# Kernel optimization log

Hardware: AMD Instinct MI355X
Metric: run time of the kernel (lower is better)

## Reference

```python
import jax, jax.numpy as jnp
import numpy as np

N = 262144   # query points
M = 4096     # boundary points
D = 128      # d_model (m)
H = 4        # num_heads
HD = D // H  # head_dim = 32
L = 3        # num_layers
PI = float(np.pi)


def multi_feature_encoding(x):
    # x: [T, 2] -> [T, 30]; 15 fixed feature maps, hstacked
    feats = [
        x,
        x ** 2,
        (x - 1.5) ** 2,
        (x - 4.5) ** 2,
        jax.nn.sigmoid(x),
        jax.nn.sigmoid(x - 1.5),
        jax.nn.sigmoid(x - 4.5),
        x - 1.5,
        x - 4.5,
        jnp.sin(PI * x),
        jnp.cos(PI * x),
        jnp.sin(PI * x * 0.25),
        jnp.cos(PI * x * 0.25),
        jnp.sin(PI * x * 0.5),
        jnp.cos(PI * x * 0.5),
    ]
    return jnp.concatenate(feats, axis=-1)


def pos_encode(x, w, b):
    # w: [30, D], b: [D]
    return jnp.sin(multi_feature_encoding(x) @ w + b)


def setup_inputs() -> dict:
    key = jax.random.key(0)
    ks = jax.random.split(key, 24)
    s = 0.05

    def p(k, shape):
        return jax.random.normal(k, shape, dtype=jnp.float32) * s

    return {
        "query_pts": jax.random.normal(ks[0], (N, 2), dtype=jnp.float32),
        "boundary_pts": jax.random.normal(ks[1], (M, 2), dtype=jnp.float32),
        # positional encoders (query / boundary)
        "pe_w": p(ks[2], (30, D)), "pe_b": p(ks[3], (D,)),
        "bpe_w": p(ks[4], (30, D)), "bpe_b": p(ks[5], (D,)),
        # per-layer per-head q/k/v projections, stacked: [L, H, D, HD]
        "Wq": p(ks[6], (L, H, D, HD)), "bq": p(ks[7], (L, H, HD)),
        "Wk": p(ks[8], (L, H, D, HD)), "bk": p(ks[9], (L, H, HD)),
        "Wv": p(ks[10], (L, H, D, HD)), "bv": p(ks[11], (L, H, HD)),
        # attention out proj and FFN (two D->D linears) per layer
        "Wo": p(ks[12], (L, D, D)), "bo": p(ks[13], (L, D)),
        "W1": p(ks[14], (L, D, D)), "b1": p(ks[15], (L, D)),
        "W2": p(ks[16], (L, D, D)), "b2": p(ks[17], (L, D)),
        # final projector: D -> D//2 -> 3
        "pw1": p(ks[18], (D, D // 2)), "pb1": p(ks[19], (D // 2,)),
        "pw2": p(ks[20], (D // 2, 3)), "pb2": p(ks[21], (3,)),
    }


def reference(query_pts, boundary_pts, pe_w, pe_b, bpe_w, bpe_b,
              Wq, bq, Wk, bk, Wv, bv, Wo, bo, W1, b1, W2, b2,
              pw1, pb1, pw2, pb2):
    h = pos_encode(query_pts, pe_w, pe_b)[None]        # [1, N, D]
    b_enc = pos_encode(boundary_pts, bpe_w, bpe_b)[None]  # [1, M, D]

    for l in range(L):
        # batched per-head projections (equivalent to the per-head Linear loop)
        qh = jnp.einsum('btd,hde->bhte', h, Wq[l]) + bq[l][None, :, None, :]
        kh = jnp.einsum('btd,hde->bhte', b_enc, Wk[l]) + bk[l][None, :, None, :]
        vh = jnp.einsum('btd,hde->bhte', b_enc, Wv[l]) + bv[l][None, :, None, :]
        qh = qh ** 2  # squared feature map
        kh = kh ** 2
        kv_sum = jnp.einsum('bhnd,bhne->bhde', kh, vh)          # [1,H,HD,HD]
        z = 1.0 / (jnp.einsum('bhnd,bhd->bhn', qh, kh.sum(axis=2)) + 1e-6)
        attn = jnp.einsum('bhnd,bhde,bhn->bhne', qh, kv_sum, z)  # [1,H,N,HD]
        attn = attn.transpose(0, 2, 1, 3).reshape(1, -1, D)      # [1,N,D]
        attn = attn @ Wo[l] + bo[l]
        x = h + attn
        ff = jax.nn.gelu(x @ W1[l] + b1[l], approximate=False) @ W2[l] + b2[l]
        h = x + ff

    out = jax.nn.gelu(h @ pw1 + pb1, approximate=False) @ pw2 + pb2  # [1,N,3]
    return out[0]  # squeeze(0) -> [N, 3]
```

## Files before the change

### kernel.cpp

```cpp
#include <hip/hip_runtime.h>
#include <hip/hip_bf16.h>

__device__ __forceinline__ float b2f(unsigned short u) {
    return __uint_as_float(((unsigned)u) << 16);
}
__device__ __forceinline__ unsigned short f2b(float f) {
    __hip_bfloat16 h = __float2bfloat16(f);
    return *reinterpret_cast<unsigned short*>(&h);
}
__device__ __forceinline__ unsigned short f2b_rne(float f) {
    unsigned u = __float_as_uint(f);
    return (unsigned short)((u + 0x7fffu + ((u >> 16) & 1u)) >> 16);
}
__device__ __forceinline__ unsigned pk_bf16(float lo, float hi) {
    unsigned r;
    asm("v_cvt_pk_bf16_f32 %0, %1, %2" : "=v"(r) : "v"(lo), "v"(hi));
    return r;
}
__device__ __forceinline__ float sigm(float v) {
    return 1.f / (1.f + __expf(-v));
}
__device__ __forceinline__ float gelu_t(float x) {
    float y = 0.7978845608f * (x + 0.044715f * x * x * x);
    float e = __expf(2.f * y);
    float th = 1.f - 2.f / (e + 1.f);
    return 0.5f * x * (1.f + th);
}

typedef __attribute__((ext_vector_type(8))) short s8v;
typedef __attribute__((ext_vector_type(4))) float f4v;

#define MFMA_BF16 __builtin_amdgcn_mfma_f32_16x16x32_bf16

__device__ __forceinline__ void make_feats(const unsigned short* __restrict__ qpts,
                                           int r, float* __restrict__ f) {
    unsigned pq = *(const unsigned*)(qpts + (size_t)r * 2);
    float x0 = b2f((unsigned short)(pq & 0xffff));
    float x1 = b2f((unsigned short)(pq >> 16));
    const float PI = 3.14159265358979323846f;
    float a0 = x0 - 1.5f, a1 = x1 - 1.5f, c0 = x0 - 4.5f, c1 = x1 - 4.5f;
    f[0] = x0;        f[1] = x1;
    f[2] = x0 * x0;   f[3] = x1 * x1;
    f[4] = a0 * a0;   f[5] = a1 * a1;
    f[6] = c0 * c0;   f[7] = c1 * c1;
    f[8] = sigm(x0);  f[9] = sigm(x1);
    f[10] = sigm(a0); f[11] = sigm(a1);
    f[12] = sigm(c0); f[13] = sigm(c1);
    f[14] = a0;       f[15] = a1;
    f[16] = c0;       f[17] = c1;
    f[18] = __sinf(PI * x0);          f[19] = __sinf(PI * x1);
    f[20] = __cosf(PI * x0);          f[21] = __cosf(PI * x1);
    f[22] = __sinf(PI * 0.25f * x0);  f[23] = __sinf(PI * 0.25f * x1);
    f[24] = __cosf(PI * 0.25f * x0);  f[25] = __cosf(PI * 0.25f * x1);
    f[26] = __sinf(PI * 0.5f * x0);   f[27] = __sinf(PI * 0.5f * x1);
    f[28] = __cosf(PI * 0.5f * x0);   f[29] = __cosf(PI * 0.5f * x1);
}

__device__ __forceinline__ void feats8(unsigned pq, int qd, float* __restrict__ f8) {
    float x0 = b2f((unsigned short)(pq & 0xffff));
    float x1 = b2f((unsigned short)(pq >> 16));
    const float PI = 3.14159265358979323846f;
    float a0 = x0 - 1.5f, a1 = x1 - 1.5f, c0 = x0 - 4.5f, c1 = x1 - 4.5f;
    if (qd == 0) {
        f8[0] = x0;      f8[1] = x1;
        f8[2] = x0 * x0; f8[3] = x1 * x1;
        f8[4] = a0 * a0; f8[5] = a1 * a1;
        f8[6] = c0 * c0; f8[7] = c1 * c1;
    } else if (qd == 1) {
        f8[0] = sigm(x0); f8[1] = sigm(x1);
        f8[2] = sigm(a0); f8[3] = sigm(a1);
        f8[4] = sigm(c0); f8[5] = sigm(c1);
        f8[6] = a0;       f8[7] = a1;
    } else if (qd == 2) {
        f8[0] = c0; f8[1] = c1;
        f8[2] = __sinf(PI * x0);          f8[3] = __sinf(PI * x1);
        f8[4] = __cosf(PI * x0);          f8[5] = __cosf(PI * x1);
        f8[6] = __sinf(PI * 0.25f * x0);  f8[7] = __sinf(PI * 0.25f * x1);
    } else {
        f8[0] = __cosf(PI * 0.25f * x0);  f8[1] = __cosf(PI * 0.25f * x1);
        f8[2] = __sinf(PI * 0.5f * x0);   f8[3] = __sinf(PI * 0.5f * x1);
        f8[4] = __cosf(PI * 0.5f * x0);   f8[5] = __cosf(PI * 0.5f * x1);
        f8[6] = 0.f;                      f8[7] = 0.f;
    }
}

struct ConvArgs {
    const void* p[22];
    int off[23];
};

__global__ __launch_bounds__(256) void convert_kernel(
    ConvArgs a, const unsigned short* __restrict__ pe_w_raw,
    int* __restrict__ flag, unsigned short* __restrict__ canon, int total)
{
    __shared__ int cnt;
    if (threadIdx.x == 0) cnt = 0;
    __syncthreads();
    float v = b2f(pe_w_raw[threadIdx.x * 2]);
    if (!(fabsf(v) < 1.0f)) atomicAdd(&cnt, 1);
    __syncthreads();
    int isf32 = (cnt >= 16) ? 1 : 0;
    if (blockIdx.x == 0 && threadIdx.x == 0) *flag = isf32;

    int g = blockIdx.x * 256 + threadIdx.x;
    if (g >= total) return;
    int s = 0;
    #pragma unroll
    for (int i = 1; i < 23; i++) s += (g >= a.off[i]) ? 1 : 0;
    int local = g - a.off[s];
    unsigned short r;
    if (isf32) r = f2b(((const float*)a.p[s])[local]);
    else       r = ((const unsigned short*)a.p[s])[local];
    canon[g] = r;
}

__global__ __launch_bounds__(256) void encode_kernel(
    const unsigned short* __restrict__ pts,
    const unsigned short* __restrict__ w,
    const unsigned short* __restrict__ b,
    float* __restrict__ out)
{
    __shared__ __align__(16) float wsm[30 * 128];
    __shared__ float bs[128];
    int t = threadIdx.x;
    for (int i = t; i < 30 * 128; i += 256) wsm[i] = b2f(w[i]);
    if (t < 128) bs[t] = b2f(b[t]);
    __syncthreads();

    int r = blockIdx.x * 8 + (t >> 5);
    int j = t & 31;
    float f[30];
    make_feats(pts, r, f);
    float s0 = bs[j * 4 + 0], s1 = bs[j * 4 + 1], s2 = bs[j * 4 + 2], s3 = bs[j * 4 + 3];
    #pragma unroll
    for (int ff = 0; ff < 30; ff++) {
        float4 wv = *(const float4*)&wsm[ff * 128 + j * 4];
        float fv = f[ff];
        s0 += fv * wv.x; s1 += fv * wv.y; s2 += fv * wv.z; s3 += fv * wv.w;
    }
    *(float4*)&out[(size_t)r * 128 + j * 4] =
        make_float4(__sinf(s0), __sinf(s1), __sinf(s2), __sinf(s3));
}

__global__ __launch_bounds__(256) void khvh_kernel(
    const float* __restrict__ benc,
    const unsigned short* __restrict__ Wk, const unsigned short* __restrict__ bk,
    const unsigned short* __restrict__ Wv, const unsigned short* __restrict__ bv,
    float* __restrict__ kh, float* __restrict__ vh, float* __restrict__ kvz)
{
    int g = blockIdx.x * 256 + threadIdx.x;
    if (g < 12672) kvz[g] = 0.f;
    int lh = g >> 17;
    int rem = g & 131071;
    int m = rem >> 5;
    int dd = rem & 31;
    const unsigned short* wk = Wk + lh * 4096 + dd;
    const unsigned short* wv = Wv + lh * 4096 + dd;
    const float* br = benc + (size_t)m * 128;
    float ka = 0.f, va = 0.f;
    #pragma unroll 8
    for (int c = 0; c < 128; c++) {
        float bb = br[c];
        ka += bb * b2f(wk[c * 32]);
        va += bb * b2f(wv[c * 32]);
    }
    ka += b2f(bk[lh * 32 + dd]); ka = ka * ka;
    va += b2f(bv[lh * 32 + dd]);
    kh[g] = ka; vh[g] = va;
}

__global__ __launch_bounds__(1024) void kvred_kernel(
    const float* __restrict__ kh, const float* __restrict__ vh,
    float* __restrict__ kvsum, float* __restrict__ ksum)
{
    __shared__ float khs[1024];
    __shared__ float vhs[1024];
    int t = threadIdx.x;
    int lh = blockIdx.x >> 3;
    int part = blockIdx.x & 7;
    int dd = t >> 5, ee = t & 31;
    float kva = 0.f, ksa = 0.f;
    for (int ch = 0; ch < 16; ch++) {
        int base = lh * 131072 + (part * 16 + ch) * 1024;
        khs[t] = kh[base + t];
        vhs[t] = vh[base + t];
        __syncthreads();
        #pragma unroll
        for (int i = 0; i < 32; i++) {
            float kk = khs[i * 32 + dd];
            kva += kk * vhs[i * 32 + ee];
            ksa += kk;
        }
        __syncthreads();
    }
    atomicAdd(&kvsum[lh * 1024 + dd * 32 + ee], kva);
    if (ee == 0) atomicAdd(&ksum[lh * 32 + dd], ksa);
}

__global__ __launch_bounds__(256) void prep_kernel(
    const unsigned short* __restrict__ Wq, const unsigned short* __restrict__ W1,
    const unsigned short* __restrict__ W2, const unsigned short* __restrict__ pw1,
    const float* __restrict__ kvs, const float* __restrict__ kss,
    const unsigned short* __restrict__ Wo, const unsigned short* __restrict__ pe_w,
    unsigned short* __restrict__ wqT, unsigned short* __restrict__ w1T,
    unsigned short* __restrict__ w2T, unsigned short* __restrict__ pw1T,
    unsigned short* __restrict__ waT, unsigned short* __restrict__ ksT,
    unsigned short* __restrict__ pweT)
{
    int g = blockIdx.x * 256 + threadIdx.x;
    if (g < 49152) {
        int l = g >> 14, r = g & 16383, n = r >> 7, k = r & 127;
        wqT[g] = Wq[((l * 4 + (n >> 5)) * 128 + k) * 32 + (n & 31)];
    } else if (g < 98304) {
        int q = g - 49152; int l = q >> 14, r = q & 16383, n = r >> 7, k = r & 127;
        w1T[q] = W1[(l * 128 + k) * 128 + n];
    } else if (g < 147456) {
        int q = g - 98304; int l = q >> 14, r = q & 16383, n = r >> 7, k = r & 127;
        w2T[q] = W2[(l * 128 + k) * 128 + n];
    } else if (g < 155648) {
        int q = g - 147456; int n = q >> 7, k = q & 127;
        pw1T[q] = pw1[k * 64 + n];
    } else if (g < 204800) {
        int q = g - 155648; int l = q >> 14, r = q & 16383, n = r >> 7, k = r & 127;
        int hk = k >> 5, dk = k & 31;
        const float* kvp = kvs + (l * 4 + hk) * 1024 + dk * 32;
        const unsigned short* wop = Wo + (size_t)(l * 128 + hk * 32) * 128 + n;
        float s = 0.f;
        #pragma unroll 8
        for (int j = 0; j < 32; j++) s += kvp[j] * b2f(wop[j * 128]);
        waT[q] = f2b(s);
    } else if (g < 210944) {
        int q = g - 204800; int l = q >> 11, r = q & 2047, n = r >> 7, k = r & 127;
        unsigned short v = 0;
        if (n < 4 && (k >> 5) == n) v = f2b(kss[(l * 4 + n) * 32 + (k & 31)]);
        ksT[q] = v;
    } else if (g < 215040) {
        int q = g - 210944; int n = q >> 5, k = q & 31;
        pweT[q] = (k < 30) ? pe_w[k * 128 + n] : (unsigned short)0;
    }
}


template<int ITERS>
__device__ __forceinline__ void stage_w(const unsigned short* __restrict__ g,
                                        unsigned short* __restrict__ wbuf, int t) {
    #pragma unroll
    for (int i = 0; i < ITERS; i++) {
        int lin = (i * 256 + t) * 16;
        s8v v = *(const s8v*)((const char*)g + lin);
        int sw = lin ^ ((((lin >> 8)) & 7) << 4);
        *(s8v*)((char*)wbuf + sw) = v;
    }
}

__device__ __forceinline__ s8v wfrag(const unsigned short* __restrict__ wbuf,
                                     int nt, int k, int l16, int qd) {
    int lin = (nt << 12) + (l16 << 8) + (k << 6) + (qd << 4);
    return *(const s8v*)((const char*)wbuf + (lin ^ ((l16 & 7) << 4)));
}

#define RUN_MM_L(AF, ...) do {                                                \
    _Pragma("unroll")                                                         \
    for (int _p = 0; _p < 4; _p++) {                                          \
        f4v _x0 = {0.f,0.f,0.f,0.f}, _x1 = {0.f,0.f,0.f,0.f};                 \
        f4v _y0 = {0.f,0.f,0.f,0.f}, _y1 = {0.f,0.f,0.f,0.f};                 \
        _Pragma("unroll")                                                     \
        for (int _k = 0; _k < 4; _k++) {                                      \
            s8v _wa = wfrag(wbuf, _p * 2,     _k, l16, qd);                   \
            s8v _wb = wfrag(wbuf, _p * 2 + 1, _k, l16, qd);                   \
            _x0 = MFMA_BF16(_wa, AF[0][_k], _x0, 0, 0, 0);                    \
            _x1 = MFMA_BF16(_wa, AF[1][_k], _x1, 0, 0, 0);                    \
            _y0 = MFMA_BF16(_wb, AF[0][_k], _y0, 0, 0, 0);                    \
            _y1 = MFMA_BF16(_wb, AF[1][_k], _y1, 0, 0, 0);                    \
        }                                                                     \
        { const int nt = _p * 2;     const int tile = 0; const f4v x = _x0; __VA_ARGS__ } \
        { const int nt = _p * 2;     const int tile = 1; const f4v x = _x1; __VA_ARGS__ } \
        { const int nt = _p * 2 + 1; const int tile = 0; const f4v x = _y0; __VA_ARGS__ } \
        { const int nt = _p * 2 + 1; const int tile = 1; const f4v x = _y1; __VA_ARGS__ } \
    }                                                                         \
} while (0)

#define LOAD_AF(AF) do {                                                      \
    _Pragma("unroll")                                                         \
    for (int _t2 = 0; _t2 < 2; _t2++)                                         \
        _Pragma("unroll")                                                     \
        for (int _k = 0; _k < 4; _k++)                                        \
            AF[_t2][_k] = *(const s8v*)(sAB + (rA0 + _t2 * 16) * 256 +        \
                                        (((_k * 64) + (qd * 16)) ^ swzA));    \
} while (0)

__global__ __launch_bounds__(256) void mega_kernel(
    const unsigned short* __restrict__ qpts,
    const unsigned short* __restrict__ pweT,
    const unsigned short* __restrict__ pe_b,
    const unsigned short* __restrict__ wqT,
    const unsigned short* __restrict__ waT,
    const unsigned short* __restrict__ ksT,
    const unsigned short* __restrict__ w1T,
    const unsigned short* __restrict__ w2T,
    const unsigned short* __restrict__ bq,
    const unsigned short* __restrict__ bo,
    const unsigned short* __restrict__ b1,
    const unsigned short* __restrict__ b2,
    const unsigned short* __restrict__ pw1T,
    const unsigned short* __restrict__ pb1,
    const unsigned short* __restrict__ pw2,
    const unsigned short* __restrict__ pb2,
    void* __restrict__ outv, const int* __restrict__ flag)
{
    __shared__ __align__(16) unsigned short sA[128 * 128];
    __shared__ __align__(16) unsigned short wbuf[16384];
    __shared__ __align__(16) float biasAll[12 * 128];
    __shared__ __align__(16) float pebs[128];
    __shared__ __align__(16) float pb1s[64];
    __shared__ float w2s[192];
    __shared__ float pb2s[3];

    int t = threadIdx.x;
    int wvi = t >> 6, ln = t & 63, qd = ln >> 4, l16 = ln & 15;
    int qd4 = qd * 4;
    int row0 = blockIdx.x * 128;
    int rA0 = wvi * 32 + l16;
    const int swzA = (l16 & 7) << 4;
    char* sAB = (char*)sA;

    for (int i = t; i < 1536; i += 256) {
        int l = i >> 9, rem = i & 511, which = rem >> 7, c = rem & 127;
        const unsigned short* bsrc = (which == 0) ? bq : (which == 1) ? bo
                                   : (which == 2) ? b1 : b2;
        biasAll[i] = b2f(bsrc[l * 128 + c]);
    }
    if (t < 128) pebs[t] = b2f(pe_b[t]);
    if (t < 64)  pb1s[t] = b2f(pb1[t]);
    if (t < 192) w2s[t] = b2f(pw2[t]);
    if (t < 3)   pb2s[t] = b2f(pb2[t]);
    __syncthreads();

    stage_w<8>(wqT, wbuf, t);

    float hres[2][8][4];

    {
        unsigned pq0 = *(const unsigned*)(qpts + (size_t)(row0 + rA0) * 2);
        unsigned pq1 = *(const unsigned*)(qpts + (size_t)(row0 + rA0 + 16) * 2);
        s8v ae0, ae1;
        {
            float f8[8]; feats8(pq0, qd, f8);
            unsigned* au = (unsigned*)&ae0;
            #pragma unroll
            for (int jj = 0; jj < 4; jj++) au[jj] = pk_bf16(f8[2 * jj], f8[2 * jj + 1]);
        }
        {
            float f8[8]; feats8(pq1, qd, f8);
            unsigned* au = (unsigned*)&ae1;
            #pragma unroll
            for (int jj = 0; jj < 4; jj++) au[jj] = pk_bf16(f8[2 * jj], f8[2 * jj + 1]);
        }
        const unsigned short* pb = pweT + l16 * 32 + qd * 8;
        #pragma unroll
        for (int nt = 0; nt < 8; nt++) {
            s8v aw = *(const s8v*)(pb + nt * 512);
            f4v x0 = {0.f, 0.f, 0.f, 0.f}, x1 = {0.f, 0.f, 0.f, 0.f};
            x0 = MFMA_BF16(aw, ae0, x0, 0, 0, 0);
            x1 = MFMA_BF16(aw, ae1, x1, 0, 0, 0);
            float4 bb = *(const float4*)&pebs[nt * 16 + qd4];
            float h0 = __sinf(x0[0] + bb.x), h1 = __sinf(x0[1] + bb.y);
            float h2 = __sinf(x0[2] + bb.z), h3 = __sinf(x0[3] + bb.w);
            hres[0][nt][0] = h0; hres[0][nt][1] = h1;
            hres[0][nt][2] = h2; hres[0][nt][3] = h3;
            uint2 pk0; pk0.x = pk_bf16(h0, h1); pk0.y = pk_bf16(h2, h3);
            *(uint2*)(sAB + rA0 * 256 + ((nt * 32 + qd * 8) ^ swzA)) = pk0;
            float g0 = __sinf(x1[0] + bb.x), g1 = __sinf(x1[1] + bb.y);
            float g2 = __sinf(x1[2] + bb.z), g3 = __sinf(x1[3] + bb.w);
            hres[1][nt][0] = g0; hres[1][nt][1] = g1;
            hres[1][nt][2] = g2; hres[1][nt][3] = g3;
            uint2 pk1; pk1.x = pk_bf16(g0, g1); pk1.y = pk_bf16(g2, g3);
            *(uint2*)(sAB + (rA0 + 16) * 256 + ((nt * 32 + qd * 8) ^ swzA)) = pk1;
        }
    }

    s8v af[2][4];

    for (int l = 0; l < 3; l++) {
        const float* bql = &biasAll[(l * 4 + 0) * 128];
        const float* bol = &biasAll[(l * 4 + 1) * 128];
        const float* b1l = &biasAll[(l * 4 + 2) * 128];
        const float* b2l = &biasAll[(l * 4 + 3) * 128];

        LOAD_AF(af);
        __syncthreads();
        if (l > 0) {  }
        RUN_MM_L(af, {
            float4 bb = *(const float4*)&bql[nt * 16 + qd4];
            float v0 = x[0] + bb.x, v1 = x[1] + bb.y;
            float v2 = x[2] + bb.z, v3 = x[3] + bb.w;
            uint2 pk; pk.x = pk_bf16(v0 * v0, v1 * v1); pk.y = pk_bf16(v2 * v2, v3 * v3);
            *(uint2*)(sAB + (rA0 + tile * 16) * 256 + ((nt * 32 + qd * 8) ^ swzA)) = pk;
        });

        LOAD_AF(af);
        s8v kf[4];
        {
            const unsigned short* kb = ksT + l * 2048 + l16 * 128 + qd * 8;
            #pragma unroll
            for (int ks = 0; ks < 4; ks++) kf[ks] = *(const s8v*)(kb + ks * 32);
        }
        __syncthreads();
        stage_w<8>(waT + l * 16384, wbuf, t);
        #pragma unroll
        for (int tile = 0; tile < 2; tile++) {
            f4v d = {0.f, 0.f, 0.f, 0.f};
            #pragma unroll
            for (int ks = 0; ks < 4; ks++) d = MFMA_BF16(kf[ks], af[tile][ks], d, 0, 0, 0);
            #pragma unroll
            for (int ks = 0; ks < 4; ks++) {
                float z = 1.f / (__shfl(d[ks], l16) + 1e-6f);
                unsigned* u = (unsigned*)&af[tile][ks];
                #pragma unroll
                for (int jj = 0; jj < 4; jj++) {
                    unsigned w = u[jj];
                    float lo = __uint_as_float(w << 16) * z;
                    float hi = __uint_as_float(w & 0xffff0000u) * z;
                    u[jj] = pk_bf16(lo, hi);
                }
            }
        }
        __syncthreads();

        RUN_MM_L(af, {
            float4 bb = *(const float4*)&bol[nt * 16 + qd4];
            float v0 = hres[tile][nt][0] + x[0] + bb.x;
            float v1 = hres[tile][nt][1] + x[1] + bb.y;
            float v2 = hres[tile][nt][2] + x[2] + bb.z;
            float v3 = hres[tile][nt][3] + x[3] + bb.w;
            hres[tile][nt][0] = v0; hres[tile][nt][1] = v1;
            hres[tile][nt][2] = v2; hres[tile][nt][3] = v3;
            uint2 pk; pk.x = pk_bf16(v0, v1); pk.y = pk_bf16(v2, v3);
            *(uint2*)(sAB + (rA0 + tile * 16) * 256 + ((nt * 32 + qd * 8) ^ swzA)) = pk;
        });

        LOAD_AF(af);
        __syncthreads();
        stage_w<8>(w1T + l * 16384, wbuf, t);
        __syncthreads();
        RUN_MM_L(af, {
            float4 bb = *(const float4*)&b1l[nt * 16 + qd4];
            uint2 pk;
            pk.x = pk_bf16(gelu_t(x[0] + bb.x), gelu_t(x[1] + bb.y));
            pk.y = pk_bf16(gelu_t(x[2] + bb.z), gelu_t(x[3] + bb.w));
            *(uint2*)(sAB + (rA0 + tile * 16) * 256 + ((nt * 32 + qd * 8) ^ swzA)) = pk;
        });

        LOAD_AF(af);
        __syncthreads();
        stage_w<8>(w2T + l * 16384, wbuf, t);
        __syncthreads();
        RUN_MM_L(af, {
            float4 bb = *(const float4*)&b2l[nt * 16 + qd4];
            float v0 = hres[tile][nt][0] + x[0] + bb.x;
            float v1 = hres[tile][nt][1] + x[1] + bb.y;
            float v2 = hres[tile][nt][2] + x[2] + bb.z;
            float v3 = hres[tile][nt][3] + x[3] + bb.w;
            hres[tile][nt][0] = v0; hres[tile][nt][1] = v1;
            hres[tile][nt][2] = v2; hres[tile][nt][3] = v3;
            uint2 pk; pk.x = pk_bf16(v0, v1); pk.y = pk_bf16(v2, v3);
            *(uint2*)(sAB + (rA0 + tile * 16) * 256 + ((nt * 32 + qd * 8) ^ swzA)) = pk;
        });

        LOAD_AF(af);
        __syncthreads();
        if (l < 2) stage_w<8>(wqT + (l + 1) * 16384, wbuf, t);
        else       stage_w<4>(pw1T, wbuf, t);
    }

    __syncthreads();
    {
        float* sAf = (float*)sA;
        const int fsw = (l16 & 7) << 1;
        #pragma unroll
        for (int p = 0; p < 2; p++) {
            f4v y0 = {0.f,0.f,0.f,0.f}, y1 = {0.f,0.f,0.f,0.f};
            f4v y2 = {0.f,0.f,0.f,0.f}, y3 = {0.f,0.f,0.f,0.f};
            #pragma unroll
            for (int ks = 0; ks < 4; ks++) {
                s8v wA = wfrag(wbuf, p * 2,     ks, l16, qd);
                s8v wB = wfrag(wbuf, p * 2 + 1, ks, l16, qd);
                y0 = MFMA_BF16(wA, af[0][ks], y0, 0, 0, 0);
                y1 = MFMA_BF16(wA, af[1][ks], y1, 0, 0, 0);
                y2 = MFMA_BF16(wB, af[0][ks], y2, 0, 0, 0);
                y3 = MFMA_BF16(wB, af[1][ks], y3, 0, 0, 0);
            }
            int n0 = (p * 2) * 16 + qd4, n1 = (p * 2 + 1) * 16 + qd4;
            float4 bA = *(const float4*)&pb1s[n0];
            float4 bB = *(const float4*)&pb1s[n1];
            int f0 = ((p * 2) * 4 + qd) ^ fsw, f1 = ((p * 2 + 1) * 4 + qd) ^ fsw;
            *(float4*)&sAf[rA0 * 64 + f0 * 4] = make_float4(
                gelu_t(y0[0] + bA.x), gelu_t(y0[1] + bA.y),
                gelu_t(y0[2] + bA.z), gelu_t(y0[3] + bA.w));
            *(float4*)&sAf[(rA0 + 16) * 64 + f0 * 4] = make_float4(
                gelu_t(y1[0] + bA.x), gelu_t(y1[1] + bA.y),
                gelu_t(y1[2] + bA.z), gelu_t(y1[3] + bA.w));
            *(float4*)&sAf[rA0 * 64 + f1 * 4] = make_float4(
                gelu_t(y2[0] + bB.x), gelu_t(y2[1] + bB.y),
                gelu_t(y2[2] + bB.z), gelu_t(y2[3] + bB.w));
            *(float4*)&sAf[(rA0 + 16) * 64 + f1 * 4] = make_float4(
                gelu_t(y3[0] + bB.x), gelu_t(y3[1] + bB.y),
                gelu_t(y3[2] + bB.z), gelu_t(y3[3] + bB.w));
        }
    }
    __syncthreads();

    {
        const float* sAf = (const float*)sA;
        for (int idx = t; idx < 384; idx += 256) {
            int r = idx / 3, c = idx - r * 3;
            int rsw = (r & 7) << 1;
            float s = pb2s[c];
            #pragma unroll
            for (int jj = 0; jj < 16; jj++) {
                float4 v = *(const float4*)&sAf[r * 64 + (jj ^ rsw) * 4];
                s += v.x * w2s[(jj * 4 + 0) * 3 + c] + v.y * w2s[(jj * 4 + 1) * 3 + c]
                   + v.z * w2s[(jj * 4 + 2) * 3 + c] + v.w * w2s[(jj * 4 + 3) * 3 + c];
            }
            size_t o = (size_t)(row0 + r) * 3 + c;
            if (*flag) ((float*)outv)[o] = s;
            else       ((unsigned short*)outv)[o] = f2b(s);
        }
    }
}

extern "C" void kernel_launch(void* const* d_in, const int* in_sizes, int n_in,
                              void* d_out, int out_size, void* d_ws, size_t ws_size,
                              hipStream_t stream) {
    const int N = in_sizes[0] / 2;
    const int M = in_sizes[1] / 2;

    ConvArgs ca;
    int total = 0;
    for (int i = 0; i < 22; i++) { ca.p[i] = d_in[i]; ca.off[i] = total; total += in_sizes[i]; }
    ca.off[22] = total;

    float* ws = (float*)d_ws;
    int* flag = (int*)ws;
    unsigned short* canon = (unsigned short*)(ws + 16);
    size_t canonF = ((size_t)(total + 1) / 2 + 15) & ~(size_t)15;
    float* b_enc = ws + 16 + canonF;
    float* khb   = b_enc + (size_t)M * 128;
    float* vhb   = khb + (size_t)12 * M * 32;
    float* kvs   = vhb + (size_t)12 * M * 32;
    float* kss   = kvs + 12288;
    unsigned short* wqT  = (unsigned short*)(kss + 384);
    unsigned short* waT  = wqT + 49152;
    unsigned short* w1T  = waT + 49152;
    unsigned short* w2T  = w1T + 49152;
    unsigned short* ksT  = w2T + 49152;
    unsigned short* pw1T = ksT + 6144;
    unsigned short* pweT = pw1T + 8192;

    const unsigned short* c_qpts = canon + ca.off[0];
    const unsigned short* c_bpts = canon + ca.off[1];
    const unsigned short* c_pew  = canon + ca.off[2];
    const unsigned short* c_peb  = canon + ca.off[3];
    const unsigned short* c_bpew = canon + ca.off[4];
    const unsigned short* c_bpeb = canon + ca.off[5];
    const unsigned short* c_Wq   = canon + ca.off[6];
    const unsigned short* c_bq   = canon + ca.off[7];
    const unsigned short* c_Wk   = canon + ca.off[8];
    const unsigned short* c_bk   = canon + ca.off[9];
    const unsigned short* c_Wv   = canon + ca.off[10];
    const unsigned short* c_bv   = canon + ca.off[11];
    const unsigned short* c_Wo   = canon + ca.off[12];
    const unsigned short* c_bo   = canon + ca.off[13];
    const unsigned short* c_W1   = canon + ca.off[14];
    const unsigned short* c_b1   = canon + ca.off[15];
    const unsigned short* c_W2   = canon + ca.off[16];
    const unsigned short* c_b2   = canon + ca.off[17];
    const unsigned short* c_pw1  = canon + ca.off[18];
    const unsigned short* c_pb1  = canon + ca.off[19];
    const unsigned short* c_pw2  = canon + ca.off[20];
    const unsigned short* c_pb2  = canon + ca.off[21];

    convert_kernel<<<(total + 255) / 256, 256, 0, stream>>>(
        ca, (const unsigned short*)d_in[2], flag, canon, total);

    encode_kernel<<<M / 8, 256, 0, stream>>>(c_bpts, c_bpew, c_bpeb, b_enc);
    khvh_kernel<<<(12 * M * 32) / 256, 256, 0, stream>>>(
        b_enc, c_Wk, c_bk, c_Wv, c_bv, khb, vhb, kvs);
    kvred_kernel<<<96, 1024, 0, stream>>>(khb, vhb, kvs, kss);
    prep_kernel<<<215040 / 256, 256, 0, stream>>>(
        c_Wq, c_W1, c_W2, c_pw1, kvs, kss, c_Wo, c_pew,
        wqT, w1T, w2T, pw1T, waT, ksT, pweT);

    mega_kernel<<<N / 128, 256, 0, stream>>>(
        c_qpts, pweT, c_peb, wqT, waT, ksT, w1T, w2T,
        c_bq, c_bo, c_b1, c_b2, pw1T, c_pb1, c_pw2, c_pb2, d_out, flag);
}
```

Baseline: 421.4 us.

## Keep activations in registers by permuting weight columns to match MFMA fragments

The weight output columns are permuted in the prep kernel (fmap) so each MFMA accumulator layout lines up directly with the B-operand fragment layout of the next matmul. Activations then stay packed in registers between layers instead of going through a shared-memory tile with its extra barriers. Weight staging becomes a global-to-register prefetch that overlaps compute before the LDS write. The final projector is fused into register FMAs plus cross-lane shuffles, and GELU switches to a cheaper sigmoid-form tanh approximation. The risks are higher register pressure, which can lower occupancy, and a small numerical change from the new GELU form.

```diff
diff --git a/kernel.cpp b/kernel.cpp
--- a/kernel.cpp
+++ b/kernel.cpp
@@ -7,10 +7,6 @@
 __device__ __forceinline__ unsigned short f2b(float f) {
     __hip_bfloat16 h = __float2bfloat16(f);
     return *reinterpret_cast<unsigned short*>(&h);
-}
-__device__ __forceinline__ unsigned short f2b_rne(float f) {
-    unsigned u = __float_as_uint(f);
-    return (unsigned short)((u + 0x7fffu + ((u >> 16) & 1u)) >> 16);
 }
 __device__ __forceinline__ unsigned pk_bf16(float lo, float hi) {
     unsigned r;
@@ -20,17 +16,28 @@
 __device__ __forceinline__ float sigm(float v) {
     return 1.f / (1.f + __expf(-v));
 }
-__device__ __forceinline__ float gelu_t(float x) {
-    float y = 0.7978845608f * (x + 0.044715f * x * x * x);
-    float e = __expf(2.f * y);
-    float th = 1.f - 2.f / (e + 1.f);
-    return 0.5f * x * (1.f + th);
+__device__ __forceinline__ float gelu_l(float x) {
+    float x2 = x * x;
+    float y2 = x * __builtin_fmaf(0.0713548163f, x2, 1.5957691216f);
+    float e  = __expf(y2);
+    float r  = __builtin_amdgcn_rcpf(e + 1.f);
+    return x - x * r;
 }
 
 typedef __attribute__((ext_vector_type(8))) short s8v;
 typedef __attribute__((ext_vector_type(4))) float f4v;
 
 #define MFMA_BF16 __builtin_amdgcn_mfma_f32_16x16x32_bf16
+
+__device__ __forceinline__ s8v mkfrag(unsigned a, unsigned b, unsigned c, unsigned d) {
+    union { unsigned u[4]; s8v v; } x;
+    x.u[0] = a; x.u[1] = b; x.u[2] = c; x.u[3] = d;
+    return x.v;
+}
+
+__device__ __forceinline__ int fmap(int s) {
+    return (s & ~31) | (((s >> 2) & 3) << 3) | (((s >> 4) & 1) << 2) | (s & 3);
+}
 
 __device__ __forceinline__ void make_feats(const unsigned short* __restrict__ qpts,
                                            int r, float* __restrict__ f) {
@@ -210,21 +217,23 @@
     int g = blockIdx.x * 256 + threadIdx.x;
     if (g < 49152) {
         int l = g >> 14, r = g & 16383, n = r >> 7, k = r & 127;
-        wqT[g] = Wq[((l * 4 + (n >> 5)) * 128 + k) * 32 + (n & 31)];
+        int na = fmap(n);
+        wqT[g] = Wq[((l * 4 + (na >> 5)) * 128 + k) * 32 + (na & 31)];
     } else if (g < 98304) {
         int q = g - 49152; int l = q >> 14, r = q & 16383, n = r >> 7, k = r & 127;
-        w1T[q] = W1[(l * 128 + k) * 128 + n];
+        w1T[q] = W1[(l * 128 + k) * 128 + fmap(n)];
     } else if (g < 147456) {
         int q = g - 98304; int l = q >> 14, r = q & 16383, n = r >> 7, k = r & 127;
-        w2T[q] = W2[(l * 128 + k) * 128 + n];
+        w2T[q] = W2[(l * 128 + k) * 128 + fmap(n)];
     } else if (g < 155648) {
         int q = g - 147456; int n = q >> 7, k = q & 127;
         pw1T[q] = pw1[k * 64 + n];
     } else if (g < 204800) {
         int q = g - 155648; int l = q >> 14, r = q & 16383, n = r >> 7, k = r & 127;
+        int na = fmap(n);
         int hk = k >> 5, dk = k & 31;
         const float* kvp = kvs + (l * 4 + hk) * 1024 + dk * 32;
-        const unsigned short* wop = Wo + (size_t)(l * 128 + hk * 32) * 128 + n;
+        const unsigned short* wop = Wo + (size_t)(l * 128 + hk * 32) * 128 + na;
         float s = 0.f;
         #pragma unroll 8
         for (int j = 0; j < 32; j++) s += kvp[j] * b2f(wop[j * 128]);
@@ -236,20 +245,26 @@
         ksT[q] = v;
     } else if (g < 215040) {
         int q = g - 210944; int n = q >> 5, k = q & 31;
-        pweT[q] = (k < 30) ? pe_w[k * 128 + n] : (unsigned short)0;
+        pweT[q] = (k < 30) ? pe_w[k * 128 + fmap(n)] : (unsigned short)0;
     }
 }
 
 
 template<int ITERS>
-__device__ __forceinline__ void stage_w(const unsigned short* __restrict__ g,
-                                        unsigned short* __restrict__ wbuf, int t) {
+__device__ __forceinline__ void load_w(const unsigned short* __restrict__ g,
+                                       int t, s8v* __restrict__ r) {
+    #pragma unroll
+    for (int i = 0; i < ITERS; i++)
+        r[i] = *(const s8v*)((const char*)g + (size_t)(i * 256 + t) * 16);
+}
+template<int ITERS>
+__device__ __forceinline__ void write_w(unsigned short* __restrict__ wbuf,
+                                        int t, const s8v* __restrict__ r) {
     #pragma unroll
     for (int i = 0; i < ITERS; i++) {
         int lin = (i * 256 + t) * 16;
-        s8v v = *(const s8v*)((const char*)g + lin);
-        int sw = lin ^ ((((lin >> 8)) & 7) << 4);
-        *(s8v*)((char*)wbuf + sw) = v;
+        int sw = lin ^ (((lin >> 8) & 7) << 4);
+        *(s8v*)((char*)wbuf + sw) = r[i];
     }
 }
 
@@ -259,35 +274,35 @@
     return *(const s8v*)((const char*)wbuf + (lin ^ ((l16 & 7) << 4)));
 }
 
-#define RUN_MM_L(AF, ...) do {                                                \
+#define MM_BODY(EPI...) do {                                                  \
+    s8v bf0[4], bf1[4];                                                       \
+    _Pragma("unroll")                                                         \
+    for (int _s = 0; _s < 4; _s++) {                                          \
+        bf0[_s] = mkfrag(pkd[0][2*_s][0], pkd[0][2*_s][1],                    \
+                         pkd[0][2*_s+1][0], pkd[0][2*_s+1][1]);               \
+        bf1[_s] = mkfrag(pkd[1][2*_s][0], pkd[1][2*_s][1],                    \
+                         pkd[1][2*_s+1][0], pkd[1][2*_s+1][1]);               \
+    }                                                                         \
     _Pragma("unroll")                                                         \
     for (int _p = 0; _p < 4; _p++) {                                          \
-        f4v _x0 = {0.f,0.f,0.f,0.f}, _x1 = {0.f,0.f,0.f,0.f};                 \
-        f4v _y0 = {0.f,0.f,0.f,0.f}, _y1 = {0.f,0.f,0.f,0.f};                 \
+        f4v _x0 = {0.f,0.f,0.f,0.f}, _x1 = _x0, _y0 = _x0, _y1 = _x0;         \
         _Pragma("unroll")                                                     \
         for (int _k = 0; _k < 4; _k++) {                                      \
             s8v _wa = wfrag(wbuf, _p * 2,     _k, l16, qd);                   \
             s8v _wb = wfrag(wbuf, _p * 2 + 1, _k, l16, qd);                   \
-            _x0 = MFMA_BF16(_wa, AF[0][_k], _x0, 0, 0, 0);                    \
-            _x1 = MFMA_BF16(_wa, AF[1][_k], _x1, 0, 0, 0);                    \
-            _y0 = MFMA_BF16(_wb, AF[0][_k], _y0, 0, 0, 0);                    \
-            _y1 = MFMA_BF16(_wb, AF[1][_k], _y1, 0, 0, 0);                    \
+            _x0 = MFMA_BF16(_wa, bf0[_k], _x0, 0, 0, 0);                      \
+            _x1 = MFMA_BF16(_wa, bf1[_k], _x1, 0, 0, 0);                      \
+            _y0 = MFMA_BF16(_wb, bf0[_k], _y0, 0, 0, 0);                      \
+            _y1 = MFMA_BF16(_wb, bf1[_k], _y1, 0, 0, 0);                      \
         }                                                                     \
-        { const int nt = _p * 2;     const int tile = 0; const f4v x = _x0; __VA_ARGS__ } \
-        { const int nt = _p * 2;     const int tile = 1; const f4v x = _x1; __VA_ARGS__ } \
-        { const int nt = _p * 2 + 1; const int tile = 0; const f4v x = _y0; __VA_ARGS__ } \
-        { const int nt = _p * 2 + 1; const int tile = 1; const f4v x = _y1; __VA_ARGS__ } \
+        { const int nt = _p * 2;     const int tile = 0; const f4v x = _x0; EPI } \
+        { const int nt = _p * 2;     const int tile = 1; const f4v x = _x1; EPI } \
+        { const int nt = _p * 2 + 1; const int tile = 0; const f4v x = _y0; EPI } \
+        { const int nt = _p * 2 + 1; const int tile = 1; const f4v x = _y1; EPI } \
     }                                                                         \
 } while (0)
 
-#define LOAD_AF(AF) do {                                                      \
-    _Pragma("unroll")                                                         \
-    for (int _t2 = 0; _t2 < 2; _t2++)                                         \
-        _Pragma("unroll")                                                     \
-        for (int _k = 0; _k < 4; _k++)                                        \
-            AF[_t2][_k] = *(const s8v*)(sAB + (rA0 + _t2 * 16) * 256 +        \
-                                        (((_k * 64) + (qd * 16)) ^ swzA));    \
-} while (0)
+#define CBDEF int cb = ((nt >> 1) << 5) + (qd << 3) + ((nt & 1) << 2)
 
 __global__ __launch_bounds__(256) void mega_kernel(
     const unsigned short* __restrict__ qpts,
@@ -308,21 +323,17 @@
     const unsigned short* __restrict__ pb2,
     void* __restrict__ outv, const int* __restrict__ flag)
 {
-    __shared__ __align__(16) unsigned short sA[128 * 128];
     __shared__ __align__(16) unsigned short wbuf[16384];
     __shared__ __align__(16) float biasAll[12 * 128];
     __shared__ __align__(16) float pebs[128];
     __shared__ __align__(16) float pb1s[64];
-    __shared__ float w2s[192];
+    __shared__ __align__(16) float w2s4[256];
     __shared__ float pb2s[3];
 
     int t = threadIdx.x;
     int wvi = t >> 6, ln = t & 63, qd = ln >> 4, l16 = ln & 15;
-    int qd4 = qd * 4;
     int row0 = blockIdx.x * 128;
     int rA0 = wvi * 32 + l16;
-    const int swzA = (l16 & 7) << 4;
-    char* sAB = (char*)sA;
 
     for (int i = t; i < 1536; i += 256) {
         int l = i >> 9, rem = i & 511, which = rem >> 7, c = rem & 127;
@@ -332,12 +343,20 @@
     }
     if (t < 128) pebs[t] = b2f(pe_b[t]);
     if (t < 64)  pb1s[t] = b2f(pb1[t]);
-    if (t < 192) w2s[t] = b2f(pw2[t]);
-    if (t < 3)   pb2s[t] = b2f(pb2[t]);
+    if (t < 64) {
+        w2s4[t * 4 + 0] = b2f(pw2[t * 3 + 0]);
+        w2s4[t * 4 + 1] = b2f(pw2[t * 3 + 1]);
+        w2s4[t * 4 + 2] = b2f(pw2[t * 3 + 2]);
+        w2s4[t * 4 + 3] = 0.f;
+    }
+    if (t < 3) pb2s[t] = b2f(pb2[t]);
     __syncthreads();
 
-    stage_w<8>(wqT, wbuf, t);
-
+    s8v sreg[8];
+    load_w<8>(wqT, t, sreg);
+    write_w<8>(wbuf, t, sreg);
+
+    unsigned pkd[2][8][2];
     float hres[2][8][4];
 
     {
@@ -363,23 +382,23 @@
             f4v x0 = {0.f, 0.f, 0.f, 0.f}, x1 = {0.f, 0.f, 0.f, 0.f};
             x0 = MFMA_BF16(aw, ae0, x0, 0, 0, 0);
             x1 = MFMA_BF16(aw, ae1, x1, 0, 0, 0);
-            float4 bb = *(const float4*)&pebs[nt * 16 + qd4];
+            CBDEF;
+            float4 bb = *(const float4*)&pebs[cb];
             float h0 = __sinf(x0[0] + bb.x), h1 = __sinf(x0[1] + bb.y);
             float h2 = __sinf(x0[2] + bb.z), h3 = __sinf(x0[3] + bb.w);
             hres[0][nt][0] = h0; hres[0][nt][1] = h1;
             hres[0][nt][2] = h2; hres[0][nt][3] = h3;
-            uint2 pk0; pk0.x = pk_bf16(h0, h1); pk0.y = pk_bf16(h2, h3);
-            *(uint2*)(sAB + rA0 * 256 + ((nt * 32 + qd * 8) ^ swzA)) = pk0;
+            pkd[0][nt][0] = pk_bf16(h0, h1);
+            pkd[0][nt][1] = pk_bf16(h2, h3);
             float g0 = __sinf(x1[0] + bb.x), g1 = __sinf(x1[1] + bb.y);
             float g2 = __sinf(x1[2] + bb.z), g3 = __sinf(x1[3] + bb.w);
             hres[1][nt][0] = g0; hres[1][nt][1] = g1;
             hres[1][nt][2] = g2; hres[1][nt][3] = g3;
-            uint2 pk1; pk1.x = pk_bf16(g0, g1); pk1.y = pk_bf16(g2, g3);
-            *(uint2*)(sAB + (rA0 + 16) * 256 + ((nt * 32 + qd * 8) ^ swzA)) = pk1;
-        }
-    }
-
-    s8v af[2][4];
+            pkd[1][nt][0] = pk_bf16(g0, g1);
+            pkd[1][nt][1] = pk_bf16(g2, g3);
+        }
+    }
+    __syncthreads();
 
     for (int l = 0; l < 3; l++) {
         const float* bql = &biasAll[(l * 4 + 0) * 128];
@@ -387,144 +406,165 @@
         const float* b1l = &biasAll[(l * 4 + 2) * 128];
         const float* b2l = &biasAll[(l * 4 + 3) * 128];
 
-        LOAD_AF(af);
-        __syncthreads();
-        if (l > 0) {  }
-        RUN_MM_L(af, {
-            float4 bb = *(const float4*)&bql[nt * 16 + qd4];
+        MM_BODY({
+            CBDEF;
+            float4 bb = *(const float4*)&bql[cb];
             float v0 = x[0] + bb.x, v1 = x[1] + bb.y;
             float v2 = x[2] + bb.z, v3 = x[3] + bb.w;
-            uint2 pk; pk.x = pk_bf16(v0 * v0, v1 * v1); pk.y = pk_bf16(v2 * v2, v3 * v3);
-            *(uint2*)(sAB + (rA0 + tile * 16) * 256 + ((nt * 32 + qd * 8) ^ swzA)) = pk;
+            pkd[tile][nt][0] = pk_bf16(v0 * v0, v1 * v1);
+            pkd[tile][nt][1] = pk_bf16(v2 * v2, v3 * v3);
         });
 
-        LOAD_AF(af);
         s8v kf[4];
         {
             const unsigned short* kb = ksT + l * 2048 + l16 * 128 + qd * 8;
             #pragma unroll
             for (int ks = 0; ks < 4; ks++) kf[ks] = *(const s8v*)(kb + ks * 32);
         }
-        __syncthreads();
-        stage_w<8>(waT + l * 16384, wbuf, t);
+        load_w<8>(waT + l * 16384, t, sreg);
         #pragma unroll
         for (int tile = 0; tile < 2; tile++) {
             f4v d = {0.f, 0.f, 0.f, 0.f};
             #pragma unroll
-            for (int ks = 0; ks < 4; ks++) d = MFMA_BF16(kf[ks], af[tile][ks], d, 0, 0, 0);
+            for (int ks = 0; ks < 4; ks++) {
+                s8v b = mkfrag(pkd[tile][2 * ks][0], pkd[tile][2 * ks][1],
+                               pkd[tile][2 * ks + 1][0], pkd[tile][2 * ks + 1][1]);
+                d = MFMA_BF16(kf[ks], b, d, 0, 0, 0);
+            }
             #pragma unroll
             for (int ks = 0; ks < 4; ks++) {
                 float z = 1.f / (__shfl(d[ks], l16) + 1e-6f);
-                unsigned* u = (unsigned*)&af[tile][ks];
                 #pragma unroll
-                for (int jj = 0; jj < 4; jj++) {
-                    unsigned w = u[jj];
-                    float lo = __uint_as_float(w << 16) * z;
-                    float hi = __uint_as_float(w & 0xffff0000u) * z;
-                    u[jj] = pk_bf16(lo, hi);
+                for (int h2 = 0; h2 < 2; h2++) {
+                    #pragma unroll
+                    for (int j = 0; j < 2; j++) {
+                        unsigned w = pkd[tile][2 * ks + h2][j];
+                        float lo = __uint_as_float(w << 16) * z;
+                        float hi = __uint_as_float(w & 0xffff0000u) * z;
+                        pkd[tile][2 * ks + h2][j] = pk_bf16(lo, hi);
+                    }
                 }
             }
         }
         __syncthreads();
-
-        RUN_MM_L(af, {
-            float4 bb = *(const float4*)&bol[nt * 16 + qd4];
+        write_w<8>(wbuf, t, sreg);
+        __syncthreads();
+
+        MM_BODY({
+            CBDEF;
+            float4 bb = *(const float4*)&bol[cb];
             float v0 = hres[tile][nt][0] + x[0] + bb.x;
             float v1 = hres[tile][nt][1] + x[1] + bb.y;
             float v2 = hres[tile][nt][2] + x[2] + bb.z;
             float v3 = hres[tile][nt][3] + x[3] + bb.w;
             hres[tile][nt][0] = v0; hres[tile][nt][1] = v1;
             hres[tile][nt][2] = v2; hres[tile][nt][3] = v3;
-            uint2 pk; pk.x = pk_bf16(v0, v1); pk.y = pk_bf16(v2, v3);
-            *(uint2*)(sAB + (rA0 + tile * 16) * 256 + ((nt * 32 + qd * 8) ^ swzA)) = pk;
+            pkd[tile][nt][0] = pk_bf16(v0, v1);
+            pkd[tile][nt][1] = pk_bf16(v2, v3);
         });
-
-        LOAD_AF(af);
-        __syncthreads();
-        stage_w<8>(w1T + l * 16384, wbuf, t);
-        __syncthreads();
-        RUN_MM_L(af, {
-            float4 bb = *(const float4*)&b1l[nt * 16 + qd4];
-            uint2 pk;
-            pk.x = pk_bf16(gelu_t(x[0] + bb.x), gelu_t(x[1] + bb.y));
-            pk.y = pk_bf16(gelu_t(x[2] + bb.z), gelu_t(x[3] + bb.w));
-            *(uint2*)(sAB + (rA0 + tile * 16) * 256 + ((nt * 32 + qd * 8) ^ swzA)) = pk;
+        load_w<8>(w1T + l * 16384, t, sreg);
+        __syncthreads();
+        write_w<8>(wbuf, t, sreg);
+        __syncthreads();
+
+        MM_BODY({
+            CBDEF;
+            float4 bb = *(const float4*)&b1l[cb];
+            float g0 = gelu_l(x[0] + bb.x), g1 = gelu_l(x[1] + bb.y);
+            float g2 = gelu_l(x[2] + bb.z), g3 = gelu_l(x[3] + bb.w);
+            pkd[tile][nt][0] = pk_bf16(g0, g1);
+            pkd[tile][nt][1] = pk_bf16(g2, g3);
         });
-
-        LOAD_AF(af);
-        __syncthreads();
-        stage_w<8>(w2T + l * 16384, wbuf, t);
-        __syncthreads();
-        RUN_MM_L(af, {
-            float4 bb = *(const float4*)&b2l[nt * 16 + qd4];
+        load_w<8>(w2T + l * 16384, t, sreg);
+        __syncthreads();
+        write_w<8>(wbuf, t, sreg);
+        __syncthreads();
+
+        MM_BODY({
+            CBDEF;
+            float4 bb = *(const float4*)&b2l[cb];
             float v0 = hres[tile][nt][0] + x[0] + bb.x;
             float v1 = hres[tile][nt][1] + x[1] + bb.y;
             float v2 = hres[tile][nt][2] + x[2] + bb.z;
             float v3 = hres[tile][nt][3] + x[3] + bb.w;
             hres[tile][nt][0] = v0; hres[tile][nt][1] = v1;
             hres[tile][nt][2] = v2; hres[tile][nt][3] = v3;
-            uint2 pk; pk.x = pk_bf16(v0, v1); pk.y = pk_bf16(v2, v3);
-            *(uint2*)(sAB + (rA0 + tile * 16) * 256 + ((nt * 32 + qd * 8) ^ swzA)) = pk;
+            pkd[tile][nt][0] = pk_bf16(v0, v1);
+            pkd[tile][nt][1] = pk_bf16(v2, v3);
         });
-
-        LOAD_AF(af);
-        __syncthreads();
-        if (l < 2) stage_w<8>(wqT + (l + 1) * 16384, wbuf, t);
-        else       stage_w<4>(pw1T, wbuf, t);
-    }
-
-    __syncthreads();
+        if (l < 2) {
+            load_w<8>(wqT + (l + 1) * 16384, t, sreg);
+            __syncthreads();
+            write_w<8>(wbuf, t, sreg);
+        } else {
+            load_w<4>(pw1T, t, sreg);
+            __syncthreads();
+            write_w<4>(wbuf, t, sreg);
+        }
+        __syncthreads();
+    }
+
     {
-        float* sAf = (float*)sA;
-        const int fsw = (l16 & 7) << 1;
+        s8v bf0[4], bf1[4];
+        #pragma unroll
+        for (int ks = 0; ks < 4; ks++) {
+            bf0[ks] = mkfrag(pkd[0][2 * ks][0], pkd[0][2 * ks][1],
+                             pkd[0][2 * ks + 1][0], pkd[0][2 * ks + 1][1]);
+            bf1[ks] = mkfrag(pkd[1][2 * ks][0], pkd[1][2 * ks][1],
+                             pkd[1][2 * ks + 1][0], pkd[1][2 * ks + 1][1]);
+        }
+        float pt0[3] = {0.f, 0.f, 0.f}, pt1[3] = {0.f, 0.f, 0.f};
         #pragma unroll
         for (int p = 0; p < 2; p++) {
-            f4v y0 = {0.f,0.f,0.f,0.f}, y1 = {0.f,0.f,0.f,0.f};
-            f4v y2 = {0.f,0.f,0.f,0.f}, y3 = {0.f,0.f,0.f,0.f};
+            f4v y00 = {0.f,0.f,0.f,0.f}, y01 = y00, y10 = y00, y11 = y00;
             #pragma unroll
             for (int ks = 0; ks < 4; ks++) {
-                s8v wA = wfrag(wbuf, p * 2,     ks, l16, qd);
-                s8v wB = wfrag(wbuf, p * 2 + 1, ks, l16, qd);
-                y0 = MFMA_BF16(wA, af[0][ks], y0, 0, 0, 0);
-                y1 = MFMA_BF16(wA, af[1][ks], y1, 0, 0, 0);
-                y2 = MFMA_BF16(wB, af[0][ks], y2, 0, 0, 0);
-                y3 = MFMA_BF16(wB, af[1][ks], y3, 0, 0, 0);
+                s8v wa = wfrag(wbuf, p * 2,     ks, l16, qd);
+                s8v wb = wfrag(wbuf, p * 2 + 1, ks, l16, qd);
+                y00 = MFMA_BF16(wa, bf0[ks], y00, 0, 0, 0);
+                y01 = MFMA_BF16(wa, bf1[ks], y01, 0, 0, 0);
+                y10 = MFMA_BF16(wb, bf0[ks], y10, 0, 0, 0);
+                y11 = MFMA_BF16(wb, bf1[ks], y11, 0, 0, 0);
             }
-            int n0 = (p * 2) * 16 + qd4, n1 = (p * 2 + 1) * 16 + qd4;
-            float4 bA = *(const float4*)&pb1s[n0];
-            float4 bB = *(const float4*)&pb1s[n1];
-            int f0 = ((p * 2) * 4 + qd) ^ fsw, f1 = ((p * 2 + 1) * 4 + qd) ^ fsw;
-            *(float4*)&sAf[rA0 * 64 + f0 * 4] = make_float4(
-                gelu_t(y0[0] + bA.x), gelu_t(y0[1] + bA.y),
-                gelu_t(y0[2] + bA.z), gelu_t(y0[3] + bA.w));
-            *(float4*)&sAf[(rA0 + 16) * 64 + f0 * 4] = make_float4(
-                gelu_t(y1[0] + bA.x), gelu_t(y1[1] + bA.y),
-                gelu_t(y1[2] + bA.z), gelu_t(y1[3] + bA.w));
-            *(float4*)&sAf[rA0 * 64 + f1 * 4] = make_float4(
-                gelu_t(y2[0] + bB.x), gelu_t(y2[1] + bB.y),
-                gelu_t(y2[2] + bB.z), gelu_t(y2[3] + bB.w));
-            *(float4*)&sAf[(rA0 + 16) * 64 + f1 * 4] = make_float4(
-                gelu_t(y3[0] + bB.x), gelu_t(y3[1] + bB.y),
-                gelu_t(y3[2] + bB.z), gelu_t(y3[3] + bB.w));
-        }
-    }
-    __syncthreads();
-
-    {
-        const float* sAf = (const float*)sA;
-        for (int idx = t; idx < 384; idx += 256) {
-            int r = idx / 3, c = idx - r * 3;
-            int rsw = (r & 7) << 1;
-            float s = pb2s[c];
             #pragma unroll
-            for (int jj = 0; jj < 16; jj++) {
-                float4 v = *(const float4*)&sAf[r * 64 + (jj ^ rsw) * 4];
-                s += v.x * w2s[(jj * 4 + 0) * 3 + c] + v.y * w2s[(jj * 4 + 1) * 3 + c]
-                   + v.z * w2s[(jj * 4 + 2) * 3 + c] + v.w * w2s[(jj * 4 + 3) * 3 + c];
+            for (int e = 0; e < 2; e++) {
+                int c0 = (p * 2 + e) * 16 + qd * 4;
+                float4 bb = *(const float4*)&pb1s[c0];
+                f4v ya = e ? y10 : y00;
+                f4v yb = e ? y11 : y01;
+                #pragma unroll
+                for (int i = 0; i < 4; i++) {
+                    float bbi = (i == 0) ? bb.x : (i == 1) ? bb.y : (i == 2) ? bb.z : bb.w;
+                    float4 w = *(const float4*)&w2s4[(c0 + i) * 4];
+                    float ga = gelu_l(ya[i] + bbi);
+                    float gb = gelu_l(yb[i] + bbi);
+                    pt0[0] = fmaf(ga, w.x, pt0[0]);
+                    pt0[1] = fmaf(ga, w.y, pt0[1]);
+                    pt0[2] = fmaf(ga, w.z, pt0[2]);
+                    pt1[0] = fmaf(gb, w.x, pt1[0]);
+                    pt1[1] = fmaf(gb, w.y, pt1[1]);
+                    pt1[2] = fmaf(gb, w.z, pt1[2]);
+                }
             }
-            size_t o = (size_t)(row0 + r) * 3 + c;
-            if (*flag) ((float*)outv)[o] = s;
-            else       ((unsigned short*)outv)[o] = f2b(s);
+        }
+        #pragma unroll
+        for (int c = 0; c < 3; c++) {
+            pt0[c] += __shfl_xor(pt0[c], 16); pt0[c] += __shfl_xor(pt0[c], 32);
+            pt1[c] += __shfl_xor(pt1[c], 16); pt1[c] += __shfl_xor(pt1[c], 32);
+            pt0[c] += pb2s[c]; pt1[c] += pb2s[c];
+        }
+        if (ln < 16) {
+            size_t r0 = (size_t)(row0 + rA0) * 3;
+            size_t r1 = (size_t)(row0 + rA0 + 16) * 3;
+            if (*flag) {
+                float* o = (float*)outv;
+                o[r0] = pt0[0]; o[r0 + 1] = pt0[1]; o[r0 + 2] = pt0[2];
+                o[r1] = pt1[0]; o[r1 + 1] = pt1[1]; o[r1 + 2] = pt1[2];
+            } else {
+                unsigned short* o = (unsigned short*)outv;
+                o[r0] = f2b(pt0[0]); o[r0 + 1] = f2b(pt0[1]); o[r0 + 2] = f2b(pt0[2]);
+                o[r1] = f2b(pt1[0]); o[r1 + 1] = f2b(pt1[1]); o[r1 + 2] = f2b(pt1[2]);
+            }
         }
     }
 }
```

New measurement: 415.1 us. About the same (-1.5%).
